# Optimization experiments

Hardware: AMD Instinct MI355X
Metric: run time of the kernel (lower is better)

## Reference

```python
import jax, jax.numpy as jnp
import numpy as np

B = 64            # decoding sequences (1 query token each)
H = 32            # query heads
HKV = 8           # kv heads (GQA)
D = 128           # head dim
BS = 16           # block size (tokens per cache block)
BPB = 64          # blocks per sequence
L = BS * BPB      # max kv length = 1024
NBLK = B * BPB    # total cache blocks = 4096
SCALE = 0.08838834764831845  # 1/sqrt(128)


def setup_inputs() -> dict:
    key = jax.random.key(0)
    k1, k2, k3, k4, k5, k6 = jax.random.split(key, 6)
    q = jax.random.normal(k1, (B, H * D), dtype=jnp.float32)
    k = jax.random.normal(k2, (B, HKV * D), dtype=jnp.float32)
    v = jax.random.normal(k3, (B, HKV * D), dtype=jnp.float32)
    k_cache = jax.random.normal(k4, (NBLK, BS, HKV, D), dtype=jnp.float32)
    v_cache = jax.random.normal(k5, (NBLK, BS, HKV, D), dtype=jnp.float32)
    # each sequence owns a disjoint run of blocks
    block_tables = jnp.arange(B * BPB, dtype=jnp.int64).reshape(B, BPB)
    # context length includes the newly stored token; at least 1
    context_lens = jax.random.randint(k6, (B,), 1, L + 1).astype(jnp.int64)
    # slot of the newest token at position context_len-1
    pos = context_lens - 1
    slot_mapping = block_tables[jnp.arange(B), pos // BS] * BS + pos % BS
    return {"q": q, "k": k, "v": v, "k_cache": k_cache, "v_cache": v_cache,
            "block_tables": block_tables, "context_lens": context_lens,
            "slot_mapping": slot_mapping}


def reference(q, k, v, k_cache, v_cache, block_tables, context_lens, slot_mapping):
    G = H // HKV
    # store new k/v into the paged cache (store_kvcache_pytorch)
    kc = k_cache.reshape(-1, HKV, D).at[slot_mapping].set(k.reshape(-1, HKV, D))
    vc = v_cache.reshape(-1, HKV, D).at[slot_mapping].set(v.reshape(-1, HKV, D))
    # block-table gather: slot(t) = block_table[t//BS]*BS + t%BS
    t = jnp.arange(L)
    slots = block_tables[:, t // BS] * BS + (t % BS)          # [B, L]
    ks = kc[slots]                                            # [B, L, HKV, D]
    vs = vc[slots]                                            # [B, L, HKV, D]
    # GQA attention: q head h uses kv head h // G
    qr = q.reshape(B, HKV, G, D)
    scores = jnp.einsum('bhgd,blhd->bhgl', qr, ks) * SCALE    # [B, HKV, G, L]
    mask = t[None, :] < context_lens[:, None]                 # [B, L]
    scores = jnp.where(mask[:, None, None, :], scores, jnp.float32(-1e30))
    p = jax.nn.softmax(scores, axis=-1)
    o = jnp.einsum('bhgl,blhd->bhgd', p, vs)                  # [B, HKV, G, D]
    return o.reshape(B, H * D)
```

## Files before the change

### kernel.cpp

```cpp
#include <hip/hip_runtime.h>

#define BB    64
#define HH    32
#define HKVH  8
#define GG    4
#define DD    128
#define BSZ   16
#define BPB   64
#define LMAX  1024
#define SCALEF 0.08838834764831845f

__device__ __forceinline__ long long ld_i(const void* p, long long i, bool is64) {
  return is64 ? ((const long long*)p)[i] : (long long)((const int*)p)[i];
}

__global__ __launch_bounds__(256, 4)
void attn_partial(const float* __restrict__ q,
                  const float* __restrict__ knew,
                  const float* __restrict__ vnew,
                  const float* __restrict__ kcache,
                  const float* __restrict__ vcache,
                  const void*  __restrict__ bt,
                  const void*  __restrict__ ctxl,
                  float* __restrict__ o_part,
                  float* __restrict__ ml_part,
                  int NP, int PART)
{
  const int part = blockIdx.x;
  const int kvh  = blockIdx.y;
  const int b    = blockIdx.z;
  const int tid  = threadIdx.x;
  const int lane = tid & 63;
  const int wave = tid >> 6;
  const int gi   = lane >> 4;
  const int j    = lane & 15;
  const int group = wave * 4 + gi;

  const bool is64 = (((const int*)bt)[1] == 0);
  const int ctx = (int)ld_i(ctxl, b, is64);

  const int pbase = part * PART;
  int nt = ctx - pbase;
  if (nt > PART) nt = PART;

  if (nt <= 0) {
    if (tid < GG) {
      const size_t pidx = (((size_t)b * HKVH + kvh) * NP + part) * GG + tid;
      ml_part[pidx * 2]     = -1e30f;
      ml_part[pidx * 2 + 1] = 0.f;
    }
    return;
  }

  const float* qb = q + ((size_t)b * HH + (size_t)kvh * GG) * DD + j * 8;
  float4 q0[GG], q1[GG];
#pragma unroll
  for (int g = 0; g < GG; ++g) {
    float4 a = *(const float4*)(qb + g * DD);
    float4 c = *(const float4*)(qb + g * DD + 4);
    a.x *= SCALEF; a.y *= SCALEF; a.z *= SCALEF; a.w *= SCALEF;
    c.x *= SCALEF; c.y *= SCALEF; c.z *= SCALEF; c.w *= SCALEF;
    q0[g] = a; q1[g] = c;
  }

  float m[GG], lsum[GG];
  float4 o0[GG], o1[GG];
#pragma unroll
  for (int g = 0; g < GG; ++g) {
    m[g] = -1e30f; lsum[g] = 0.f;
    o0[g] = make_float4(0.f, 0.f, 0.f, 0.f);
    o1[g] = make_float4(0.f, 0.f, 0.f, 0.f);
  }

  const int iters = (nt + 15) >> 4;
  const int ctxm1 = ctx - 1;
  const float* newrow_k = knew + ((size_t)b * HKVH + kvh) * DD;
  const float* newrow_v = vnew + ((size_t)b * HKVH + kvh) * DD;
  const long long btrow = (long long)b * BPB + (pbase >> 4);

  const float* kr; const float* vr;
  {
    const int t = pbase + group;
    const long long blk = ld_i(bt, btrow, is64);
    const size_t off = (((size_t)blk * BSZ + group) * HKVH + kvh) * DD;
    kr = (t >= ctxm1) ? newrow_k : kcache + off;
    vr = (t >= ctxm1) ? newrow_v : vcache + off;
  }
  float4 ka = *(const float4*)(kr + j * 8);
  float4 kb = *(const float4*)(kr + j * 8 + 4);
  float4 va = *(const float4*)(vr + j * 8);
  float4 vb = *(const float4*)(vr + j * 8 + 4);

  for (int it = 0; it < iters; ++it) {
    const int itn = (it + 1 < iters) ? it + 1 : it;
    const int tn = pbase + itn * 16 + group;
    const long long blkn = ld_i(bt, btrow + itn, is64);
    const size_t offn = (((size_t)blkn * BSZ + group) * HKVH + kvh) * DD;
    const float* nkr = (tn >= ctxm1) ? newrow_k : kcache + offn;
    const float* nvr = (tn >= ctxm1) ? newrow_v : vcache + offn;
    const float4 nka = *(const float4*)(nkr + j * 8);
    const float4 nkb = *(const float4*)(nkr + j * 8 + 4);
    const float4 nva = *(const float4*)(nvr + j * 8);
    const float4 nvb = *(const float4*)(nvr + j * 8 + 4);

    const int t = pbase + it * 16 + group;
    if (t < ctx) {
      float s[GG];
#pragma unroll
      for (int g = 0; g < GG; ++g) {
        s[g] = q0[g].x * ka.x + q0[g].y * ka.y + q0[g].z * ka.z + q0[g].w * ka.w
             + q1[g].x * kb.x + q1[g].y * kb.y + q1[g].z * kb.z + q1[g].w * kb.w;
      }
#pragma unroll
      for (int off = 8; off >= 1; off >>= 1) {
#pragma unroll
        for (int g = 0; g < GG; ++g) s[g] += __shfl_xor(s[g], off, 16);
      }
#pragma unroll
      for (int g = 0; g < GG; ++g) {
        const float sg = s[g];
        const float mo = m[g];
        const float mn = fmaxf(mo, sg);
        const float p  = __expf(sg - mn);
        if (mn > mo) {
          const float al = __expf(mo - mn);
          lsum[g] *= al;
          o0[g].x *= al; o0[g].y *= al; o0[g].z *= al; o0[g].w *= al;
          o1[g].x *= al; o1[g].y *= al; o1[g].z *= al; o1[g].w *= al;
        }
        m[g] = mn;
        lsum[g] += p;
        o0[g].x += p * va.x; o0[g].y += p * va.y; o0[g].z += p * va.z; o0[g].w += p * va.w;
        o1[g].x += p * vb.x; o1[g].y += p * vb.y; o1[g].z += p * vb.z; o1[g].w += p * vb.w;
      }
    }
    ka = nka; kb = nkb; va = nva; vb = nvb;
  }

#pragma unroll
  for (int off = 16; off <= 32; off <<= 1) {
#pragma unroll
    for (int g = 0; g < GG; ++g) {
      const float m2 = __shfl_xor(m[g], off);
      const float l2 = __shfl_xor(lsum[g], off);
      float4 p0, p1;
      p0.x = __shfl_xor(o0[g].x, off); p0.y = __shfl_xor(o0[g].y, off);
      p0.z = __shfl_xor(o0[g].z, off); p0.w = __shfl_xor(o0[g].w, off);
      p1.x = __shfl_xor(o1[g].x, off); p1.y = __shfl_xor(o1[g].y, off);
      p1.z = __shfl_xor(o1[g].z, off); p1.w = __shfl_xor(o1[g].w, off);
      const float mn = fmaxf(m[g], m2);
      const float w1 = __expf(m[g] - mn);
      const float w2 = __expf(m2 - mn);
      m[g] = mn;
      lsum[g] = lsum[g] * w1 + l2 * w2;
      o0[g].x = o0[g].x * w1 + p0.x * w2; o0[g].y = o0[g].y * w1 + p0.y * w2;
      o0[g].z = o0[g].z * w1 + p0.z * w2; o0[g].w = o0[g].w * w1 + p0.w * w2;
      o1[g].x = o1[g].x * w1 + p1.x * w2; o1[g].y = o1[g].y * w1 + p1.y * w2;
      o1[g].z = o1[g].z * w1 + p1.z * w2; o1[g].w = o1[g].w * w1 + p1.w * w2;
    }
  }

  __shared__ float sm_o[4][GG][DD];
  __shared__ float sm_ml[4][GG][2];
  if (gi == 0) {
#pragma unroll
    for (int g = 0; g < GG; ++g) {
      *(float4*)&sm_o[wave][g][j * 8]     = o0[g];
      *(float4*)&sm_o[wave][g][j * 8 + 4] = o1[g];
    }
    if (j == 0) {
#pragma unroll
      for (int g = 0; g < GG; ++g) { sm_ml[wave][g][0] = m[g]; sm_ml[wave][g][1] = lsum[g]; }
    }
  }
  __syncthreads();

#pragma unroll
  for (int rep = 0; rep < 2; ++rep) {
    const int idx = tid + rep * 256;
    const int g = idx >> 7;
    const int d = idx & 127;
    float M = -1e30f;
#pragma unroll
    for (int s2 = 0; s2 < 4; ++s2) M = fmaxf(M, sm_ml[s2][g][0]);
    float Ls = 0.f, Os = 0.f;
#pragma unroll
    for (int s2 = 0; s2 < 4; ++s2) {
      const float w = __expf(sm_ml[s2][g][0] - M);
      Ls += sm_ml[s2][g][1] * w;
      Os += sm_o[s2][g][d] * w;
    }
    const size_t pidx = (((size_t)b * HKVH + kvh) * NP + part) * GG + g;
    o_part[pidx * DD + d] = Os;
    if (d == 0) { ml_part[pidx * 2] = M; ml_part[pidx * 2 + 1] = Ls; }
  }
}

__global__ __launch_bounds__(256)
void attn_combine(const float* __restrict__ o_part,
                  const float* __restrict__ ml_part,
                  float* __restrict__ out, int NP)
{
  const int blk = blockIdx.x;
  const int tid = threadIdx.x;
#pragma unroll
  for (int rep = 0; rep < 2; ++rep) {
    const int idx = tid + rep * 256;
    const int g = idx >> 7;
    const int d = idx & 127;
    const size_t base = (size_t)blk * NP;
    float M = -1e30f;
    for (int p = 0; p < NP; ++p)
      M = fmaxf(M, ml_part[((base + p) * GG + g) * 2]);
    float Ls = 0.f, Os = 0.f;
    for (int p = 0; p < NP; ++p) {
      const size_t pidx = (base + p) * GG + g;
      const float mp = ml_part[pidx * 2];
      if (mp > -1e29f) {
        const float w = __expf(mp - M);
        Ls += ml_part[pidx * 2 + 1] * w;
        Os += o_part[pidx * DD + d] * w;
      }
    }
    out[(size_t)blk * GG * DD + g * DD + d] = Os / Ls;
  }
}

extern "C" void kernel_launch(void* const* d_in, const int* in_sizes, int n_in,
                              void* d_out, int out_size, void* d_ws, size_t ws_size,
                              hipStream_t stream)
{
  const float* q  = (const float*)d_in[0];
  const float* kn = (const float*)d_in[1];
  const float* vn = (const float*)d_in[2];
  const float* kc = (const float*)d_in[3];
  const float* vc = (const float*)d_in[4];
  const void*  bt = d_in[5];
  const void*  cl = d_in[6];
  float* out = (float*)d_out;

  int NP = 8;
  while (NP > 1) {
    size_t need = (size_t)BB * HKVH * NP * GG * (DD + 2) * sizeof(float);
    if (need <= ws_size) break;
    NP >>= 1;
  }
  const int PART = LMAX / NP;

  float* o_part  = (float*)d_ws;
  float* ml_part = o_part + (size_t)BB * HKVH * NP * GG * DD;

  dim3 grid1(NP, HKVH, BB);
  attn_partial<<<grid1, 256, 0, stream>>>(q, kn, vn, kc, vc, bt, cl,
                                          o_part, ml_part, NP, PART);
  attn_combine<<<BB * HKVH, 256, 0, stream>>>(o_part, ml_part, out, NP);
}
```

Baseline: 494.6 us.

## Rework partial attention loop: 32-lane rows, 128-token chunks, unrolled independent loads

Each token row is now handled by 32 lanes with one float4 per lane instead of 16 lanes with two, so a wave covers 2 tokens per step. The loop walks 128-token chunks, preloads 8 block-table entries, and fully unrolls 16 steps so the compiler can issue many independent K/V loads ahead of the math, replacing the manual one-step prefetch. The online softmax rescale becomes branch-free, with masked tokens set to -1e30. This costs an extra shuffle stage per token and computes on padded tokens past the context, with loads still issued for them.

```diff
diff --git a/kernel.cpp b/kernel.cpp
--- a/kernel.cpp
+++ b/kernel.cpp
@@ -32,9 +32,9 @@
   const int tid  = threadIdx.x;
   const int lane = tid & 63;
   const int wave = tid >> 6;
-  const int gi   = lane >> 4;
-  const int j    = lane & 15;
-  const int group = wave * 4 + gi;
+  const int gi   = lane >> 5;
+  const int jj   = lane & 31;
+  const int group = wave * 2 + gi;
 
   const bool is64 = (((const int*)bt)[1] == 0);
   const int ctx = (int)ld_i(ctxl, b, is64);
@@ -52,112 +52,91 @@
     return;
   }
 
-  const float* qb = q + ((size_t)b * HH + (size_t)kvh * GG) * DD + j * 8;
-  float4 q0[GG], q1[GG];
+  const float* qb = q + ((size_t)b * HH + (size_t)kvh * GG) * DD + jj * 4;
+  float4 qf[GG];
 #pragma unroll
   for (int g = 0; g < GG; ++g) {
     float4 a = *(const float4*)(qb + g * DD);
-    float4 c = *(const float4*)(qb + g * DD + 4);
     a.x *= SCALEF; a.y *= SCALEF; a.z *= SCALEF; a.w *= SCALEF;
-    c.x *= SCALEF; c.y *= SCALEF; c.z *= SCALEF; c.w *= SCALEF;
-    q0[g] = a; q1[g] = c;
+    qf[g] = a;
   }
 
   float m[GG], lsum[GG];
-  float4 o0[GG], o1[GG];
+  float4 o[GG];
 #pragma unroll
   for (int g = 0; g < GG; ++g) {
     m[g] = -1e30f; lsum[g] = 0.f;
-    o0[g] = make_float4(0.f, 0.f, 0.f, 0.f);
-    o1[g] = make_float4(0.f, 0.f, 0.f, 0.f);
-  }
-
-  const int iters = (nt + 15) >> 4;
+    o[g] = make_float4(0.f, 0.f, 0.f, 0.f);
+  }
+
   const int ctxm1 = ctx - 1;
-  const float* newrow_k = knew + ((size_t)b * HKVH + kvh) * DD;
-  const float* newrow_v = vnew + ((size_t)b * HKVH + kvh) * DD;
-  const long long btrow = (long long)b * BPB + (pbase >> 4);
-
-  const float* kr; const float* vr;
-  {
-    const int t = pbase + group;
-    const long long blk = ld_i(bt, btrow, is64);
-    const size_t off = (((size_t)blk * BSZ + group) * HKVH + kvh) * DD;
-    kr = (t >= ctxm1) ? newrow_k : kcache + off;
-    vr = (t >= ctxm1) ? newrow_v : vcache + off;
-  }
-  float4 ka = *(const float4*)(kr + j * 8);
-  float4 kb = *(const float4*)(kr + j * 8 + 4);
-  float4 va = *(const float4*)(vr + j * 8);
-  float4 vb = *(const float4*)(vr + j * 8 + 4);
-
-  for (int it = 0; it < iters; ++it) {
-    const int itn = (it + 1 < iters) ? it + 1 : it;
-    const int tn = pbase + itn * 16 + group;
-    const long long blkn = ld_i(bt, btrow + itn, is64);
-    const size_t offn = (((size_t)blkn * BSZ + group) * HKVH + kvh) * DD;
-    const float* nkr = (tn >= ctxm1) ? newrow_k : kcache + offn;
-    const float* nvr = (tn >= ctxm1) ? newrow_v : vcache + offn;
-    const float4 nka = *(const float4*)(nkr + j * 8);
-    const float4 nkb = *(const float4*)(nkr + j * 8 + 4);
-    const float4 nva = *(const float4*)(nvr + j * 8);
-    const float4 nvb = *(const float4*)(nvr + j * 8 + 4);
-
-    const int t = pbase + it * 16 + group;
-    if (t < ctx) {
+  const float* newrow_k = knew + ((size_t)b * HKVH + kvh) * DD + jj * 4;
+  const float* newrow_v = vnew + ((size_t)b * HKVH + kvh) * DD + jj * 4;
+
+  const int pend = pbase + PART;
+  for (int cb = pbase; cb < pend; cb += 128) {
+    if (cb >= ctx) break;
+    const long long btrow = (long long)b * BPB + (cb >> 4);
+    int btv[8];
+#pragma unroll
+    for (int i = 0; i < 8; ++i) btv[i] = (int)ld_i(bt, btrow + i, is64);
+
+#pragma unroll
+    for (int it = 0; it < 16; ++it) {
+      const int t   = cb + it * 8 + group;
+      const int blk = btv[it >> 1];
+      const unsigned off =
+        (((unsigned)blk * BSZ + (unsigned)(t & 15)) * HKVH + (unsigned)kvh) * DD
+        + (unsigned)jj * 4;
+      const float* kr = (t >= ctxm1) ? newrow_k : kcache + off;
+      const float* vr = (t >= ctxm1) ? newrow_v : vcache + off;
+      const float4 kf = *(const float4*)kr;
+      const float4 vf = *(const float4*)vr;
+
       float s[GG];
 #pragma unroll
       for (int g = 0; g < GG; ++g) {
-        s[g] = q0[g].x * ka.x + q0[g].y * ka.y + q0[g].z * ka.z + q0[g].w * ka.w
-             + q1[g].x * kb.x + q1[g].y * kb.y + q1[g].z * kb.z + q1[g].w * kb.w;
-      }
-#pragma unroll
-      for (int off = 8; off >= 1; off >>= 1) {
-#pragma unroll
-        for (int g = 0; g < GG; ++g) s[g] += __shfl_xor(s[g], off, 16);
-      }
+        s[g] = qf[g].x * kf.x + qf[g].y * kf.y + qf[g].z * kf.z + qf[g].w * kf.w;
+      }
+#pragma unroll
+      for (int sh = 16; sh >= 1; sh >>= 1) {
+#pragma unroll
+        for (int g = 0; g < GG; ++g) s[g] += __shfl_xor(s[g], sh);
+      }
+      const bool live = (t < ctx);
 #pragma unroll
       for (int g = 0; g < GG; ++g) {
-        const float sg = s[g];
+        const float sg = live ? s[g] : -1e30f;
         const float mo = m[g];
         const float mn = fmaxf(mo, sg);
+        const float al = __expf(mo - mn);
         const float p  = __expf(sg - mn);
-        if (mn > mo) {
-          const float al = __expf(mo - mn);
-          lsum[g] *= al;
-          o0[g].x *= al; o0[g].y *= al; o0[g].z *= al; o0[g].w *= al;
-          o1[g].x *= al; o1[g].y *= al; o1[g].z *= al; o1[g].w *= al;
-        }
         m[g] = mn;
-        lsum[g] += p;
-        o0[g].x += p * va.x; o0[g].y += p * va.y; o0[g].z += p * va.z; o0[g].w += p * va.w;
-        o1[g].x += p * vb.x; o1[g].y += p * vb.y; o1[g].z += p * vb.z; o1[g].w += p * vb.w;
-      }
-    }
-    ka = nka; kb = nkb; va = nva; vb = nvb;
-  }
-
-#pragma unroll
-  for (int off = 16; off <= 32; off <<= 1) {
-#pragma unroll
-    for (int g = 0; g < GG; ++g) {
-      const float m2 = __shfl_xor(m[g], off);
-      const float l2 = __shfl_xor(lsum[g], off);
-      float4 p0, p1;
-      p0.x = __shfl_xor(o0[g].x, off); p0.y = __shfl_xor(o0[g].y, off);
-      p0.z = __shfl_xor(o0[g].z, off); p0.w = __shfl_xor(o0[g].w, off);
-      p1.x = __shfl_xor(o1[g].x, off); p1.y = __shfl_xor(o1[g].y, off);
-      p1.z = __shfl_xor(o1[g].z, off); p1.w = __shfl_xor(o1[g].w, off);
-      const float mn = fmaxf(m[g], m2);
-      const float w1 = __expf(m[g] - mn);
-      const float w2 = __expf(m2 - mn);
-      m[g] = mn;
-      lsum[g] = lsum[g] * w1 + l2 * w2;
-      o0[g].x = o0[g].x * w1 + p0.x * w2; o0[g].y = o0[g].y * w1 + p0.y * w2;
-      o0[g].z = o0[g].z * w1 + p0.z * w2; o0[g].w = o0[g].w * w1 + p0.w * w2;
-      o1[g].x = o1[g].x * w1 + p1.x * w2; o1[g].y = o1[g].y * w1 + p1.y * w2;
-      o1[g].z = o1[g].z * w1 + p1.z * w2; o1[g].w = o1[g].w * w1 + p1.w * w2;
-    }
+        lsum[g] = lsum[g] * al + p;
+        o[g].x = o[g].x * al + p * vf.x;
+        o[g].y = o[g].y * al + p * vf.y;
+        o[g].z = o[g].z * al + p * vf.z;
+        o[g].w = o[g].w * al + p * vf.w;
+      }
+    }
+  }
+
+#pragma unroll
+  for (int g = 0; g < GG; ++g) {
+    const float m2 = __shfl_xor(m[g], 32);
+    const float l2 = __shfl_xor(lsum[g], 32);
+    float4 p2;
+    p2.x = __shfl_xor(o[g].x, 32); p2.y = __shfl_xor(o[g].y, 32);
+    p2.z = __shfl_xor(o[g].z, 32); p2.w = __shfl_xor(o[g].w, 32);
+    const float mn = fmaxf(m[g], m2);
+    const float w1 = __expf(m[g] - mn);
+    const float w2 = __expf(m2 - mn);
+    m[g] = mn;
+    lsum[g] = lsum[g] * w1 + l2 * w2;
+    o[g].x = o[g].x * w1 + p2.x * w2;
+    o[g].y = o[g].y * w1 + p2.y * w2;
+    o[g].z = o[g].z * w1 + p2.z * w2;
+    o[g].w = o[g].w * w1 + p2.w * w2;
   }
 
   __shared__ float sm_o[4][GG][DD];
@@ -165,10 +144,9 @@
   if (gi == 0) {
 #pragma unroll
     for (int g = 0; g < GG; ++g) {
-      *(float4*)&sm_o[wave][g][j * 8]     = o0[g];
-      *(float4*)&sm_o[wave][g][j * 8 + 4] = o1[g];
-    }
-    if (j == 0) {
+      *(float4*)&sm_o[wave][g][jj * 4] = o[g];
+    }
+    if (jj == 0) {
 #pragma unroll
       for (int g = 0; g < GG; ++g) { sm_ml[wave][g][0] = m[g]; sm_ml[wave][g][1] = lsum[g]; }
     }
```

Result: no change. 498.9 us (+0.9%).
